# Kernel optimization log

Measured on AMD Instinct MI355X. Metric: run time of the kernel, lower is better.

## Reference

```python
import jax, jax.numpy as jnp
import numpy as np

B, D, E, H, L, T = 512, 64, 512, 1024, 2, 96
LN_EPS = 1e-5


def setup_inputs() -> dict:
    key = jax.random.key(0)
    ks = jax.random.split(key, 20)
    r = lambda k, shape, sc=0.05: (jax.random.normal(k, shape, jnp.float32) * sc)
    inp = {
        "x_0": jax.random.normal(ks[0], (B, D), jnp.float32),
        "h_n": jax.random.normal(ks[1], (L, B, H), jnp.float32) * 0.1,
        "c_n": jax.random.normal(ks[2], (L, B, H), jnp.float32) * 0.1,
        "forecast_window": T,
        # share_embedding: Linear(D -> E)
        "emb_W": r(ks[3], (D, E)),
        "emb_b": r(ks[4], (E,)),
        # LSTM layer 0: input E -> hidden H ; gates order (i, f, g, o)
        "W_ih0": r(ks[5], (E, 4 * H)),
        "W_hh0": r(ks[6], (H, 4 * H)),
        "b_ih0": r(ks[7], (4 * H,)),
        "b_hh0": r(ks[8], (4 * H,)),
        # LSTM layer 1: input H -> hidden H
        "W_ih1": r(ks[9], (H, 4 * H)),
        "W_hh1": r(ks[10], (H, 4 * H)),
        "b_ih1": r(ks[11], (4 * H,)),
        "b_hh1": r(ks[12], (4 * H,)),
        # fc: Linear(H,H) -> LayerNorm(H) -> ReLU -> Linear(H,D)
        "fc1_W": r(ks[13], (H, H)),
        "fc1_b": r(ks[14], (H,)),
        "ln_g": jnp.ones((H,), jnp.float32),
        "ln_b": jnp.zeros((H,), jnp.float32),
        "fc2_W": r(ks[15], (H, D)),
        "fc2_b": r(ks[16], (D,)),
    }
    return inp


def _lstm_cell(x, h, c, Wih, Whh, b):
    gates = x @ Wih + h @ Whh + b  # [B, 4H]
    i, f, g, o = jnp.split(gates, 4, axis=-1)
    c2 = jax.nn.sigmoid(f) * c + jax.nn.sigmoid(i) * jnp.tanh(g)
    h2 = jax.nn.sigmoid(o) * jnp.tanh(c2)
    return h2, c2


def reference(x_0, h_n, c_n, forecast_window, emb_W, emb_b,
              W_ih0, W_hh0, b_ih0, b_hh0, W_ih1, W_hh1, b_ih1, b_hh1,
              fc1_W, fc1_b, ln_g, ln_b, fc2_W, fc2_b):
    b0 = b_ih0 + b_hh0
    b1 = b_ih1 + b_hh1

    def step(carry, _):
        x, h0, c0, h1, c1 = carry
        xe = x @ emb_W + emb_b                      # embedding
        h0, c0 = _lstm_cell(xe, h0, c0, W_ih0, W_hh0, b0)
        h1, c1 = _lstm_cell(h0, h1, c1, W_ih1, W_hh1, b1)
        z = h1 @ fc1_W + fc1_b                      # Linear
        mu = jnp.mean(z, axis=-1, keepdims=True)    # LayerNorm
        var = jnp.mean((z - mu) ** 2, axis=-1, keepdims=True)
        z = (z - mu) * jax.lax.rsqrt(var + LN_EPS) * ln_g + ln_b
        y = jax.nn.relu(z) @ fc2_W + fc2_b          # ReLU -> Linear
        return (y, h0, c0, h1, c1), y

    carry0 = (x_0, h_n[0], c_n[0], h_n[1], c_n[1])
    _, ys = jax.lax.scan(step, carry0, None, length=int(forecast_window))
    return jnp.transpose(ys, (1, 0, 2))  # [B, T, D]
```

## Files before the change

kernel.cpp:

```cpp
#include <hip/hip_runtime.h>
#include <hip/hip_bf16.h>

using bf16 = __hip_bfloat16;
using short8 = __attribute__((ext_vector_type(8))) short;
using f32x4 = __attribute__((ext_vector_type(4))) float;

#define BB 512
#define HH 1024
#define DD 64
#define TT 96

__device__ __forceinline__ void load_lds16(const void* g, void* l) {
  __builtin_amdgcn_global_load_lds(
      (const __attribute__((address_space(1))) unsigned int*)g,
      (__attribute__((address_space(3))) unsigned int*)l, 16, 0, 0);
}

__device__ __forceinline__ float sigm(float x) { return 1.0f / (1.0f + __expf(-x)); }
__device__ __forceinline__ float tanh_f(float x) {
  float e = __expf(2.0f * x);
  return 1.0f - 2.0f / (e + 1.0f);
}
__device__ __forceinline__ float wred(float v) {
#pragma unroll
  for (int m = 1; m < 64; m <<= 1) v += __shfl_xor(v, m, 64);
  return v;
}


__global__ __launch_bounds__(256) void init_states_k(
    const float* __restrict__ x0, const float* __restrict__ hn, const float* __restrict__ cn,
    bf16* __restrict__ xbh, bf16* __restrict__ xbl,
    bf16* __restrict__ h0h, bf16* __restrict__ h0l,
    bf16* __restrict__ h1h, bf16* __restrict__ h1l,
    float* __restrict__ c0, float* __restrict__ c1)
{
  int i = blockIdx.x * 256 + threadIdx.x;
  if (i < BB * HH) {
    float v0 = hn[i];
    bf16 a0 = __float2bfloat16(v0);
    h0h[i] = a0; h0l[i] = __float2bfloat16(v0 - __bfloat162float(a0));
    float v1 = hn[BB * HH + i];
    bf16 a1 = __float2bfloat16(v1);
    h1h[i] = a1; h1l[i] = __float2bfloat16(v1 - __bfloat162float(a1));
    c0[i] = cn[i];
    c1[i] = cn[BB * HH + i];
  }
  if (i < BB * DD) {
    float v = x0[i];
    bf16 a = __float2bfloat16(v);
    xbh[i] = a; xbl[i] = __float2bfloat16(v - __bfloat162float(a));
  }
}

__device__ __forceinline__ int gate_perm(int c) {
  int g = c >> 10, n = c & 1023;
  return (n >> 5) * 128 + g * 32 + (n & 31);
}

__global__ __launch_bounds__(256) void fold_emb_k(
    const float* __restrict__ embW, const float* __restrict__ embB,
    const float* __restrict__ Wih0, const float* __restrict__ bih0, const float* __restrict__ bhh0,
    bf16* __restrict__ W0h, bf16* __restrict__ W0l, float* __restrict__ bias0)
{
  __shared__ float sW[512 * 8];
  __shared__ float sb[512];
  int tid = threadIdx.x;
  int d0 = blockIdx.y * 8;
  for (int i = tid; i < 4096; i += 256) {
    int j = i >> 9;
    int e = i & 511;
    sW[e * 8 + j] = embW[(size_t)(d0 + j) * 512 + e];
  }
  for (int i = tid; i < 512; i += 256) sb[i] = embB[i];
  __syncthreads();
  int c = blockIdx.x * 256 + tid;
  float acc[8] = {0, 0, 0, 0, 0, 0, 0, 0};
  float bacc = 0.0f;
  for (int e = 0; e < 512; ++e) {
    float wv = Wih0[(size_t)e * 4096 + c];
    float4 wa = *(const float4*)&sW[e * 8];
    float4 wb = *(const float4*)&sW[e * 8 + 4];
    acc[0] += wa.x * wv; acc[1] += wa.y * wv; acc[2] += wa.z * wv; acc[3] += wa.w * wv;
    acc[4] += wb.x * wv; acc[5] += wb.y * wv; acc[6] += wb.z * wv; acc[7] += wb.w * wv;
    bacc += sb[e] * wv;
  }
  int pr = gate_perm(c);
#pragma unroll
  for (int j = 0; j < 8; ++j) {
    float v = acc[j];
    bf16 h = __float2bfloat16(v);
    W0h[(size_t)pr * 1088 + d0 + j] = h;
    W0l[(size_t)pr * 1088 + d0 + j] = __float2bfloat16(v - __bfloat162float(h));
  }
  if (blockIdx.y == 0) bias0[pr] = bacc + bih0[c] + bhh0[c];
}

template <bool PERM>
__global__ __launch_bounds__(256) void transpose_conv_k(
    const float* __restrict__ src, int N,
    bf16* __restrict__ dsth, bf16* __restrict__ dstl, int dstStride, int k0)
{
  __shared__ float tb[32][33];
  int tx = threadIdx.x & 31;
  int ty = threadIdx.x >> 5;
  int c0 = blockIdx.x * 32;
  int kk0 = blockIdx.y * 32;
#pragma unroll
  for (int q = 0; q < 4; ++q) {
    int k = kk0 + q * 8 + ty;
    tb[q * 8 + ty][tx] = src[(size_t)k * N + c0 + tx];
  }
  __syncthreads();
#pragma unroll
  for (int q = 0; q < 4; ++q) {
    int cc = c0 + q * 8 + ty;
    int pr = PERM ? gate_perm(cc) : cc;
    float v = tb[tx][q * 8 + ty];
    bf16 h = __float2bfloat16(v);
    size_t di = (size_t)pr * dstStride + k0 + kk0 + tx;
    dsth[di] = h;
    dstl[di] = __float2bfloat16(v - __bfloat162float(h));
  }
}

__global__ __launch_bounds__(256) void bias_perm_k(
    const float* __restrict__ a, const float* __restrict__ b, float* __restrict__ out)
{
  int c = blockIdx.x * 256 + threadIdx.x;
  out[gate_perm(c)] = a[c] + b[c];
}

template <int EPI>
__global__ __launch_bounds__(256) void gemm_step_k(
    const bf16* __restrict__ A1h, const bf16* __restrict__ A1l, int lda1, int K1len,
    const bf16* __restrict__ A2h, const bf16* __restrict__ A2l, int lda2,
    const bf16* __restrict__ Bth, const bf16* __restrict__ Btl, int KTOT,
    const float* __restrict__ bias,
    float* __restrict__ zout,
    float* __restrict__ cstate,
    bf16* __restrict__ houth, bf16* __restrict__ houtl,
    int nPanels)
{
  __shared__ __align__(16) char smem[49152];
  const int tid = threadIdx.x;
  const int lane = tid & 63;
  const int wv = tid >> 6;
  const int bid = blockIdx.x;
  const int npanel = bid % nPanels;
  const int m0 = (bid / nPanels) * 64;
  const int nrow0 = npanel * 128;

  f32x4 acc[8] = {};
  const int ntiles = KTOT >> 5;

  auto stage = [&](int qbuf, int kt) {
    char* lb = smem + qbuf * 24576;
    {
      int row = tid >> 2, sl = tid & 3;
      int sb = (sl * 16) ^ (((row >> 2) & 3) << 4);
      int ke = kt + (sb >> 1);
      const bf16 *gh, *gl;
      if (kt < K1len) {
        gh = A1h + (size_t)(m0 + row) * lda1 + ke;
        gl = A1l + (size_t)(m0 + row) * lda1 + ke;
      } else {
        gh = A2h + (size_t)(m0 + row) * lda2 + (ke - K1len);
        gl = A2l + (size_t)(m0 + row) * lda2 + (ke - K1len);
      }
      load_lds16((const void*)gh, (void*)(lb + tid * 16));
      load_lds16((const void*)gl, (void*)(lb + 4096 + tid * 16));
    }
#pragma unroll
    for (int q = 0; q < 2; ++q) {
      int L = q * 256 + tid;
      int row = L >> 2, sl = L & 3;
      int sb = (sl * 16) ^ (((row >> 2) & 3) << 4);
      int ke = kt + (sb >> 1);
      load_lds16((const void*)(Bth + (size_t)(nrow0 + row) * KTOT + ke),
                 (void*)(lb + 8192 + L * 16));
      load_lds16((const void*)(Btl + (size_t)(nrow0 + row) * KTOT + ke),
                 (void*)(lb + 16384 + L * 16));
    }
  };

  stage(0, 0);
  __syncthreads();
  const int l15 = lane & 15;
  const int lhi = lane >> 4;
  const int kb = lhi * 16;
  const int arow = wv * 16 + l15;
  const int aoff = arow * 64 + (kb ^ (((arow >> 2) & 3) << 4));

  for (int t = 0; t < ntiles; ++t) {
    int cur = t & 1;
    if (t + 1 < ntiles) stage(cur ^ 1, (t + 1) << 5);
    const char* base = smem + cur * 24576;
    short8 ah = *(const short8*)(base + aoff);
    short8 al = *(const short8*)(base + 4096 + aoff);
#pragma unroll
    for (int f = 0; f < 8; ++f) {
      int brow = f * 16 + l15;
      int boff = brow * 64 + (kb ^ (((brow >> 2) & 3) << 4));
      short8 bh = *(const short8*)(base + 8192 + boff);
      short8 bl = *(const short8*)(base + 16384 + boff);
      acc[f] = __builtin_amdgcn_mfma_f32_16x16x32_bf16(ah, bh, acc[f], 0, 0, 0);
      acc[f] = __builtin_amdgcn_mfma_f32_16x16x32_bf16(ah, bl, acc[f], 0, 0, 0);
      acc[f] = __builtin_amdgcn_mfma_f32_16x16x32_bf16(al, bh, acc[f], 0, 0, 0);
    }
    __syncthreads();
  }

  if (EPI == 0) {
#pragma unroll
    for (int s = 0; s < 2; ++s) {
      f32x4 ai = acc[0 + s], af = acc[2 + s], ag = acc[4 + s], ao = acc[6 + s];
      int unit = npanel * 32 + s * 16 + l15;
      int prb = npanel * 128 + s * 16 + l15;
      float bi = bias[prb + 0];
      float bfv = bias[prb + 32];
      float bg = bias[prb + 64];
      float bo = bias[prb + 96];
#pragma unroll
      for (int r = 0; r < 4; ++r) {
        int row = m0 + wv * 16 + lhi * 4 + r;
        float iv = ai[r] + bi;
        float fv = af[r] + bfv;
        float gv = ag[r] + bg;
        float ov = ao[r] + bo;
        size_t idx = (size_t)row * HH + unit;
        float co = cstate[idx];
        float cn2 = sigm(fv) * co + sigm(iv) * tanh_f(gv);
        cstate[idx] = cn2;
        float hv = sigm(ov) * tanh_f(cn2);
        bf16 hh = __float2bfloat16(hv);
        houth[idx] = hh;
        houtl[idx] = __float2bfloat16(hv - __bfloat162float(hh));
      }
    }
  } else {
#pragma unroll
    for (int f = 0; f < 8; ++f) {
      int col = npanel * 128 + f * 16 + l15;
      float bb = bias[col];
#pragma unroll
      for (int r = 0; r < 4; ++r) {
        int row = m0 + wv * 16 + lhi * 4 + r;
        zout[(size_t)row * HH + col] = acc[f][r] + bb;
      }
    }
  }
}

__global__ __launch_bounds__(256) void ln_fc2_k(
    const float* __restrict__ z, const float* __restrict__ lng, const float* __restrict__ lnb,
    const float* __restrict__ W2 , const float* __restrict__ b2,
    float* __restrict__ out ,
    bf16* __restrict__ xbh, bf16* __restrict__ xbl, int tstep)
{
  __shared__ float sa[4][1024];
  __shared__ float red[4][4][64];
  int tid = threadIdx.x, lane = tid & 63, w = tid >> 6;
  int row = blockIdx.x * 4 + w;
  float zv[16];
#pragma unroll
  for (int j = 0; j < 16; ++j) zv[j] = z[(size_t)row * 1024 + j * 64 + lane];
  float s = 0;
#pragma unroll
  for (int j = 0; j < 16; ++j) s += zv[j];
  s = wred(s);
  float mu = s * (1.0f / 1024.0f);
  float vs = 0;
#pragma unroll
  for (int j = 0; j < 16; ++j) { float d = zv[j] - mu; vs += d * d; }
  vs = wred(vs);
  float rstd = rsqrtf(vs * (1.0f / 1024.0f) + 1e-5f);
#pragma unroll
  for (int j = 0; j < 16; ++j) {
    int k = j * 64 + lane;
    float a = (zv[j] - mu) * rstd * lng[k] + lnb[k];
    sa[w][k] = a > 0.0f ? a : 0.0f;
  }
  __syncthreads();
  int n = tid & 63, ks = (tid >> 6) * 256;
  float p0 = 0, p1 = 0, p2 = 0, p3 = 0;
  for (int k = ks; k < ks + 256; ++k) {
    float wv2 = W2[(size_t)k * 64 + n];
    p0 += sa[0][k] * wv2; p1 += sa[1][k] * wv2; p2 += sa[2][k] * wv2; p3 += sa[3][k] * wv2;
  }
  int sl = tid >> 6;
  red[0][sl][n] = p0; red[1][sl][n] = p1; red[2][sl][n] = p2; red[3][sl][n] = p3;
  __syncthreads();
  int rr = tid >> 6;
  float y = red[rr][0][n] + red[rr][1][n] + red[rr][2][n] + red[rr][3][n] + b2[n];
  int orow = blockIdx.x * 4 + rr;
  out[((size_t)orow * TT + tstep) * DD + n] = y;
  bf16 hh = __float2bfloat16(y);
  xbh[(size_t)orow * DD + n] = hh;
  xbl[(size_t)orow * DD + n] = __float2bfloat16(y - __bfloat162float(hh));
}


extern "C" void kernel_launch(void* const* d_in, const int* in_sizes, int n_in,
                              void* d_out, int out_size, void* d_ws, size_t ws_size,
                              hipStream_t stream)
{
  const float* x0   = (const float*)d_in[0];
  const float* hn   = (const float*)d_in[1];
  const float* cn   = (const float*)d_in[2];
  const float* embW = (const float*)d_in[4];
  const float* embB = (const float*)d_in[5];
  const float* Wih0 = (const float*)d_in[6];
  const float* Whh0 = (const float*)d_in[7];
  const float* bih0 = (const float*)d_in[8];
  const float* bhh0 = (const float*)d_in[9];
  const float* Wih1 = (const float*)d_in[10];
  const float* Whh1 = (const float*)d_in[11];
  const float* bih1 = (const float*)d_in[12];
  const float* bhh1 = (const float*)d_in[13];
  const float* fc1W = (const float*)d_in[14];
  const float* fc1b = (const float*)d_in[15];
  const float* lng  = (const float*)d_in[16];
  const float* lnb  = (const float*)d_in[17];
  const float* fc2W = (const float*)d_in[18];
  const float* fc2b = (const float*)d_in[19];

  char* wp = (char*)d_ws;
  size_t off = 0;
  auto alloc = [&](size_t bytes) -> void* {
    void* p = wp + off;
    off += (bytes + 255) & ~(size_t)255;
    return p;
  };

  bf16* W0th  = (bf16*)alloc((size_t)4096 * 1088 * 2);
  bf16* W0tl  = (bf16*)alloc((size_t)4096 * 1088 * 2);
  bf16* W1th  = (bf16*)alloc((size_t)4096 * 2048 * 2);
  bf16* W1tl  = (bf16*)alloc((size_t)4096 * 2048 * 2);
  bf16* f1h   = (bf16*)alloc((size_t)1024 * 1024 * 2);
  bf16* f1l   = (bf16*)alloc((size_t)1024 * 1024 * 2);
  float* bias0 = (float*)alloc(4096 * 4);
  float* bias1 = (float*)alloc(4096 * 4);
  bf16* xbh   = (bf16*)alloc((size_t)BB * DD * 2);
  bf16* xbl   = (bf16*)alloc((size_t)BB * DD * 2);
  bf16* h0h_a = (bf16*)alloc((size_t)BB * HH * 2);
  bf16* h0h_b = (bf16*)alloc((size_t)BB * HH * 2);
  bf16* h0l_a = (bf16*)alloc((size_t)BB * HH * 2);
  bf16* h0l_b = (bf16*)alloc((size_t)BB * HH * 2);
  bf16* h1h_a = (bf16*)alloc((size_t)BB * HH * 2);
  bf16* h1h_b = (bf16*)alloc((size_t)BB * HH * 2);
  bf16* h1l_a = (bf16*)alloc((size_t)BB * HH * 2);
  bf16* h1l_b = (bf16*)alloc((size_t)BB * HH * 2);
  float* c0   = (float*)alloc((size_t)BB * HH * 4);
  float* c1   = (float*)alloc((size_t)BB * HH * 4);
  float* z    = (float*)alloc((size_t)BB * HH * 4);

  init_states_k<<<2048, 256, 0, stream>>>(x0, hn, cn, xbh, xbl, h0h_a, h0l_a, h1h_a, h1l_a, c0, c1);
  fold_emb_k<<<dim3(16, 8), 256, 0, stream>>>(embW, embB, Wih0, bih0, bhh0, W0th, W0tl, bias0);
  transpose_conv_k<true><<<dim3(128, 32), 256, 0, stream>>>(Whh0, 4096, W0th, W0tl, 1088, 64);
  transpose_conv_k<true><<<dim3(128, 32), 256, 0, stream>>>(Wih1, 4096, W1th, W1tl, 2048, 0);
  transpose_conv_k<true><<<dim3(128, 32), 256, 0, stream>>>(Whh1, 4096, W1th, W1tl, 2048, 1024);
  transpose_conv_k<false><<<dim3(32, 32), 256, 0, stream>>>(fc1W, 1024, f1h, f1l, 1024, 0);
  bias_perm_k<<<16, 256, 0, stream>>>(bih1, bhh1, bias1);

  bf16* h0h[2] = {h0h_a, h0h_b};
  bf16* h0l[2] = {h0l_a, h0l_b};
  bf16* h1h[2] = {h1h_a, h1h_b};
  bf16* h1l[2] = {h1l_a, h1l_b};
  float* outp = (float*)d_out;

  for (int t = 0; t < TT; ++t) {
    int p = t & 1;
    gemm_step_k<0><<<256, 256, 0, stream>>>(
        xbh, xbl, DD, DD, h0h[p], h0l[p], HH, W0th, W0tl, 1088, bias0,
        nullptr, c0, h0h[p ^ 1], h0l[p ^ 1], 32);
    gemm_step_k<0><<<256, 256, 0, stream>>>(
        h0h[p ^ 1], h0l[p ^ 1], HH, HH, h1h[p], h1l[p], HH, W1th, W1tl, 2048, bias1,
        nullptr, c1, h1h[p ^ 1], h1l[p ^ 1], 32);
    gemm_step_k<1><<<64, 256, 0, stream>>>(
        h1h[p ^ 1], h1l[p ^ 1], HH, 1024, h1h[p ^ 1], h1l[p ^ 1], HH, f1h, f1l, 1024,
        fc1b, z, nullptr, nullptr, nullptr, 8);
    ln_fc2_k<<<128, 256, 0, stream>>>(z, lng, lnb, fc2W, fc2b, outp, xbh, xbl, t);
  }
}
```

Measured before the change: 10.72 ms.

## Replace per-step kernel launches with a persistent kernel using grid barriers

The 384 per-timestep launches (two LSTM gate GEMMs, fc1 GEMM, LayerNorm+fc2) are merged into one persistent kernel of 256 blocks of 128 threads. The phases are separated by a software global barrier built on atomics. The gate GEMM tiling changes to 4x4 MFMA fragments per wave, with a finer gate permutation (16-unit groups). fc1 and LN/fc2 are retiled so every phase uses the same 256 blocks. This removes launch and tail overhead, but the barrier requires all blocks to be co-resident and cuts per-block parallelism, with only 2 waves per block in most phases.

```diff
diff --git a/kernel.cpp b/kernel.cpp
--- a/kernel.cpp
+++ b/kernel.cpp
@@ -9,6 +9,7 @@
 #define HH 1024
 #define DD 64
 #define TT 96
+#define NBLK 256
 
 __device__ __forceinline__ void load_lds16(const void* g, void* l) {
   __builtin_amdgcn_global_load_lds(
@@ -25,6 +26,11 @@
 #pragma unroll
   for (int m = 1; m < 64; m <<= 1) v += __shfl_xor(v, m, 64);
   return v;
+}
+
+__device__ __forceinline__ int gate_perm(int c) {
+  int g = c >> 10, n = c & 1023;
+  return (n >> 4) * 64 + g * 16 + (n & 15);
 }
 
 
@@ -33,9 +39,10 @@
     bf16* __restrict__ xbh, bf16* __restrict__ xbl,
     bf16* __restrict__ h0h, bf16* __restrict__ h0l,
     bf16* __restrict__ h1h, bf16* __restrict__ h1l,
-    float* __restrict__ c0, float* __restrict__ c1)
+    float* __restrict__ c0, float* __restrict__ c1, unsigned* __restrict__ barp)
 {
   int i = blockIdx.x * 256 + threadIdx.x;
+  if (blockIdx.x == 0 && threadIdx.x < 128) barp[threadIdx.x] = 0u;
   if (i < BB * HH) {
     float v0 = hn[i];
     bf16 a0 = __float2bfloat16(v0);
@@ -51,11 +58,6 @@
     bf16 a = __float2bfloat16(v);
     xbh[i] = a; xbl[i] = __float2bfloat16(v - __bfloat162float(a));
   }
-}
-
-__device__ __forceinline__ int gate_perm(int c) {
-  int g = c >> 10, n = c & 1023;
-  return (n >> 5) * 128 + g * 32 + (n & 31);
 }
 
 __global__ __launch_bounds__(256) void fold_emb_k(
@@ -131,140 +133,232 @@
   out[gate_perm(c)] = a[c] + b[c];
 }
 
-template <int EPI>
-__global__ __launch_bounds__(256) void gemm_step_k(
-    const bf16* __restrict__ A1h, const bf16* __restrict__ A1l, int lda1, int K1len,
-    const bf16* __restrict__ A2h, const bf16* __restrict__ A2l, int lda2,
-    const bf16* __restrict__ Bth, const bf16* __restrict__ Btl, int KTOT,
-    const float* __restrict__ bias,
-    float* __restrict__ zout,
-    float* __restrict__ cstate,
-    bf16* __restrict__ houth, bf16* __restrict__ houtl,
-    int nPanels)
-{
-  __shared__ __align__(16) char smem[49152];
-  const int tid = threadIdx.x;
-  const int lane = tid & 63;
-  const int wv = tid >> 6;
-  const int bid = blockIdx.x;
-  const int npanel = bid % nPanels;
-  const int m0 = (bid / nPanels) * 64;
+
+struct PA {
+  bf16 *xbh, *xbl;
+  bf16 *h0h_a, *h0h_b, *h0l_a, *h0l_b;
+  bf16 *h1h_a, *h1h_b, *h1l_a, *h1l_b;
+  float *c0, *c1, *z;
+  const bf16 *W0h, *W0l, *W1h, *W1l, *F1h, *F1l;
+  const float *bias0, *bias1, *fc1b, *lng, *lnb, *W2, *b2;
+  float *out;
+  unsigned *bar;
+};
+
+__device__ __forceinline__ void gbar(unsigned* bar, int tid) {
+  __syncthreads();
+  if (tid == 0) {
+    __threadfence();
+    unsigned* gen = bar + 64;
+    unsigned g = __hip_atomic_load(gen, __ATOMIC_RELAXED, __HIP_MEMORY_SCOPE_AGENT);
+    unsigned a = __hip_atomic_fetch_add(bar, 1u, __ATOMIC_ACQ_REL, __HIP_MEMORY_SCOPE_AGENT);
+    if (a == NBLK - 1) {
+      __hip_atomic_store(bar, 0u, __ATOMIC_RELAXED, __HIP_MEMORY_SCOPE_AGENT);
+      __hip_atomic_store(gen, g + 1u, __ATOMIC_RELEASE, __HIP_MEMORY_SCOPE_AGENT);
+    } else {
+      while (__hip_atomic_load(gen, __ATOMIC_ACQUIRE, __HIP_MEMORY_SCOPE_AGENT) == g)
+        __builtin_amdgcn_s_sleep(2);
+    }
+  }
+  __syncthreads();
+}
+
+__device__ __forceinline__ void gates_phase(
+    char* smem, int bid, int tid,
+    const bf16* A1h, const bf16* A1l, int lda1, int K1len,
+    const bf16* A2h, const bf16* A2l, int lda2,
+    const bf16* Bh, const bf16* Bl, int KTOT,
+    const float* bias, float* cst, bf16* hho, bf16* hlo)
+{
+  const int lane = tid & 63, wv = tid >> 6;
+  const int npanel = bid & 31, m0 = (bid >> 5) * 64;
   const int nrow0 = npanel * 128;
-
-  f32x4 acc[8] = {};
+  const int l15 = lane & 15, lhi = lane >> 4, kb = lhi * 16;
+
+  f32x4 acc[16];
+#pragma unroll
+  for (int i = 0; i < 16; ++i) acc[i] = f32x4{0, 0, 0, 0};
+
   const int ntiles = KTOT >> 5;
 
-  auto stage = [&](int qbuf, int kt) {
-    char* lb = smem + qbuf * 24576;
+  auto stage = [&](int buf, int kt) {
+    char* lb = smem + buf * 24576;
+    bool first = kt < K1len;
+#pragma unroll
+    for (int q = 0; q < 2; ++q) {
+      int L = q * 128 + tid;
+      int row = L >> 2, sl = L & 3;
+      int sb = (sl * 16) ^ (((row >> 2) & 3) << 4);
+      int ke = kt + (sb >> 1);
+      const bf16* gh = first ? A1h + (size_t)(m0 + row) * lda1 + ke
+                             : A2h + (size_t)(m0 + row) * lda2 + (ke - K1len);
+      const bf16* gl = first ? A1l + (size_t)(m0 + row) * lda1 + ke
+                             : A2l + (size_t)(m0 + row) * lda2 + (ke - K1len);
+      load_lds16(gh, lb + L * 16);
+      load_lds16(gl, lb + 4096 + L * 16);
+    }
+#pragma unroll
+    for (int q = 0; q < 4; ++q) {
+      int L = q * 128 + tid;
+      int row = L >> 2, sl = L & 3;
+      int sb = (sl * 16) ^ (((row >> 2) & 3) << 4);
+      int ke = kt + (sb >> 1);
+      load_lds16(Bh + (size_t)(nrow0 + row) * KTOT + ke, lb + 8192 + L * 16);
+      load_lds16(Bl + (size_t)(nrow0 + row) * KTOT + ke, lb + 16384 + L * 16);
+    }
+  };
+
+  stage(0, 0);
+  __syncthreads();
+  for (int t = 0; t < ntiles; ++t) {
+    int cur = t & 1;
+    if (t + 1 < ntiles) stage(cur ^ 1, (t + 1) << 5);
+    const char* base = smem + cur * 24576;
+    short8 ah[4], al[4], bh[4], bl[4];
+#pragma unroll
+    for (int mf = 0; mf < 4; ++mf) {
+      int arow = mf * 16 + l15;
+      int aoff = arow * 64 + (kb ^ (((arow >> 2) & 3) << 4));
+      ah[mf] = *(const short8*)(base + aoff);
+      al[mf] = *(const short8*)(base + 4096 + aoff);
+    }
+#pragma unroll
+    for (int nf = 0; nf < 4; ++nf) {
+      int brow = wv * 64 + nf * 16 + l15;
+      int boff = brow * 64 + (kb ^ (((brow >> 2) & 3) << 4));
+      bh[nf] = *(const short8*)(base + 8192 + boff);
+      bl[nf] = *(const short8*)(base + 16384 + boff);
+    }
+#pragma unroll
+    for (int mf = 0; mf < 4; ++mf)
+#pragma unroll
+      for (int nf = 0; nf < 4; ++nf) {
+        f32x4 c = acc[mf * 4 + nf];
+        c = __builtin_amdgcn_mfma_f32_16x16x32_bf16(ah[mf], bh[nf], c, 0, 0, 0);
+        c = __builtin_amdgcn_mfma_f32_16x16x32_bf16(ah[mf], bl[nf], c, 0, 0, 0);
+        c = __builtin_amdgcn_mfma_f32_16x16x32_bf16(al[mf], bh[nf], c, 0, 0, 0);
+        acc[mf * 4 + nf] = c;
+      }
+    __syncthreads();
+  }
+
+  const int unit = npanel * 32 + wv * 16 + l15;
+  const int prb = npanel * 128 + wv * 64 + l15;
+  float bi = bias[prb + 0];
+  float bfv = bias[prb + 16];
+  float bg = bias[prb + 32];
+  float bo = bias[prb + 48];
+#pragma unroll
+  for (int mf = 0; mf < 4; ++mf) {
+    f32x4 ai = acc[mf * 4 + 0], af = acc[mf * 4 + 1];
+    f32x4 ag = acc[mf * 4 + 2], ao = acc[mf * 4 + 3];
+#pragma unroll
+    for (int r = 0; r < 4; ++r) {
+      int row = m0 + mf * 16 + lhi * 4 + r;
+      size_t idx = (size_t)row * HH + unit;
+      float iv = ai[r] + bi, fv = af[r] + bfv, gv = ag[r] + bg, ov = ao[r] + bo;
+      float co = cst[idx];
+      float cn2 = sigm(fv) * co + sigm(iv) * tanh_f(gv);
+      cst[idx] = cn2;
+      float hv = sigm(ov) * tanh_f(cn2);
+      bf16 hh = __float2bfloat16(hv);
+      hho[idx] = hh;
+      hlo[idx] = __float2bfloat16(hv - __bfloat162float(hh));
+    }
+  }
+}
+
+__device__ __forceinline__ void fc1_phase(
+    char* smem, int bid, int tid,
+    const bf16* Ah, const bf16* Al,
+    const bf16* Bh, const bf16* Bl,
+    const float* bias, float* z)
+{
+  const int lane = tid & 63, wv = tid >> 6;
+  const int n0 = (bid & 15) * 64, m0 = (bid >> 4) * 32;
+  const int l15 = lane & 15, lhi = lane >> 4, kb = lhi * 16;
+  f32x4 acc[4];
+#pragma unroll
+  for (int i = 0; i < 4; ++i) acc[i] = f32x4{0, 0, 0, 0};
+
+  auto stage = [&](int buf, int kt) {
+    char* lb = smem + buf * 12288;
     {
       int row = tid >> 2, sl = tid & 3;
       int sb = (sl * 16) ^ (((row >> 2) & 3) << 4);
       int ke = kt + (sb >> 1);
-      const bf16 *gh, *gl;
-      if (kt < K1len) {
-        gh = A1h + (size_t)(m0 + row) * lda1 + ke;
-        gl = A1l + (size_t)(m0 + row) * lda1 + ke;
-      } else {
-        gh = A2h + (size_t)(m0 + row) * lda2 + (ke - K1len);
-        gl = A2l + (size_t)(m0 + row) * lda2 + (ke - K1len);
-      }
-      load_lds16((const void*)gh, (void*)(lb + tid * 16));
-      load_lds16((const void*)gl, (void*)(lb + 4096 + tid * 16));
+      load_lds16(Ah + (size_t)(m0 + row) * HH + ke, lb + tid * 16);
+      load_lds16(Al + (size_t)(m0 + row) * HH + ke, lb + 2048 + tid * 16);
     }
 #pragma unroll
     for (int q = 0; q < 2; ++q) {
-      int L = q * 256 + tid;
+      int L = q * 128 + tid;
       int row = L >> 2, sl = L & 3;
       int sb = (sl * 16) ^ (((row >> 2) & 3) << 4);
       int ke = kt + (sb >> 1);
-      load_lds16((const void*)(Bth + (size_t)(nrow0 + row) * KTOT + ke),
-                 (void*)(lb + 8192 + L * 16));
-      load_lds16((const void*)(Btl + (size_t)(nrow0 + row) * KTOT + ke),
-                 (void*)(lb + 16384 + L * 16));
+      load_lds16(Bh + (size_t)(n0 + row) * HH + ke, lb + 4096 + L * 16);
+      load_lds16(Bl + (size_t)(n0 + row) * HH + ke, lb + 8192 + L * 16);
     }
   };
-
   stage(0, 0);
   __syncthreads();
-  const int l15 = lane & 15;
-  const int lhi = lane >> 4;
-  const int kb = lhi * 16;
-  const int arow = wv * 16 + l15;
-  const int aoff = arow * 64 + (kb ^ (((arow >> 2) & 3) << 4));
-
-  for (int t = 0; t < ntiles; ++t) {
+  for (int t = 0; t < 32; ++t) {
     int cur = t & 1;
-    if (t + 1 < ntiles) stage(cur ^ 1, (t + 1) << 5);
-    const char* base = smem + cur * 24576;
-    short8 ah = *(const short8*)(base + aoff);
-    short8 al = *(const short8*)(base + 4096 + aoff);
-#pragma unroll
-    for (int f = 0; f < 8; ++f) {
-      int brow = f * 16 + l15;
+    if (t + 1 < 32) stage(cur ^ 1, (t + 1) << 5);
+    const char* base = smem + cur * 12288;
+    short8 ah[2], al[2], bh[2], bl[2];
+#pragma unroll
+    for (int mf = 0; mf < 2; ++mf) {
+      int arow = mf * 16 + l15;
+      int aoff = arow * 64 + (kb ^ (((arow >> 2) & 3) << 4));
+      ah[mf] = *(const short8*)(base + aoff);
+      al[mf] = *(const short8*)(base + 2048 + aoff);
+    }
+#pragma unroll
+    for (int nf = 0; nf < 2; ++nf) {
+      int brow = wv * 32 + nf * 16 + l15;
       int boff = brow * 64 + (kb ^ (((brow >> 2) & 3) << 4));
-      short8 bh = *(const short8*)(base + 8192 + boff);
-      short8 bl = *(const short8*)(base + 16384 + boff);
-      acc[f] = __builtin_amdgcn_mfma_f32_16x16x32_bf16(ah, bh, acc[f], 0, 0, 0);
-      acc[f] = __builtin_amdgcn_mfma_f32_16x16x32_bf16(ah, bl, acc[f], 0, 0, 0);
-      acc[f] = __builtin_amdgcn_mfma_f32_16x16x32_bf16(al, bh, acc[f], 0, 0, 0);
-    }
+      bh[nf] = *(const short8*)(base + 4096 + boff);
+      bl[nf] = *(const short8*)(base + 8192 + boff);
+    }
+#pragma unroll
+    for (int mf = 0; mf < 2; ++mf)
+#pragma unroll
+      for (int nf = 0; nf < 2; ++nf) {
+        f32x4 c = acc[mf * 2 + nf];
+        c = __builtin_amdgcn_mfma_f32_16x16x32_bf16(ah[mf], bh[nf], c, 0, 0, 0);
+        c = __builtin_amdgcn_mfma_f32_16x16x32_bf16(ah[mf], bl[nf], c, 0, 0, 0);
+        c = __builtin_amdgcn_mfma_f32_16x16x32_bf16(al[mf], bh[nf], c, 0, 0, 0);
+        acc[mf * 2 + nf] = c;
+      }
     __syncthreads();
   }
-
-  if (EPI == 0) {
-#pragma unroll
-    for (int s = 0; s < 2; ++s) {
-      f32x4 ai = acc[0 + s], af = acc[2 + s], ag = acc[4 + s], ao = acc[6 + s];
-      int unit = npanel * 32 + s * 16 + l15;
-      int prb = npanel * 128 + s * 16 + l15;
-      float bi = bias[prb + 0];
-      float bfv = bias[prb + 32];
-      float bg = bias[prb + 64];
-      float bo = bias[prb + 96];
+#pragma unroll
+  for (int mf = 0; mf < 2; ++mf)
+#pragma unroll
+    for (int nf = 0; nf < 2; ++nf) {
+      int col = n0 + wv * 32 + nf * 16 + l15;
+      float bb = bias[col];
 #pragma unroll
       for (int r = 0; r < 4; ++r) {
-        int row = m0 + wv * 16 + lhi * 4 + r;
-        float iv = ai[r] + bi;
-        float fv = af[r] + bfv;
-        float gv = ag[r] + bg;
-        float ov = ao[r] + bo;
-        size_t idx = (size_t)row * HH + unit;
-        float co = cstate[idx];
-        float cn2 = sigm(fv) * co + sigm(iv) * tanh_f(gv);
-        cstate[idx] = cn2;
-        float hv = sigm(ov) * tanh_f(cn2);
-        bf16 hh = __float2bfloat16(hv);
-        houth[idx] = hh;
-        houtl[idx] = __float2bfloat16(hv - __bfloat162float(hh));
+        int row = m0 + mf * 16 + lhi * 4 + r;
+        z[(size_t)row * HH + col] = acc[mf * 2 + nf][r] + bb;
       }
     }
-  } else {
-#pragma unroll
-    for (int f = 0; f < 8; ++f) {
-      int col = npanel * 128 + f * 16 + l15;
-      float bb = bias[col];
-#pragma unroll
-      for (int r = 0; r < 4; ++r) {
-        int row = m0 + wv * 16 + lhi * 4 + r;
-        zout[(size_t)row * HH + col] = acc[f][r] + bb;
-      }
-    }
-  }
-}
-
-__global__ __launch_bounds__(256) void ln_fc2_k(
-    const float* __restrict__ z, const float* __restrict__ lng, const float* __restrict__ lnb,
-    const float* __restrict__ W2 , const float* __restrict__ b2,
-    float* __restrict__ out ,
-    bf16* __restrict__ xbh, bf16* __restrict__ xbl, int tstep)
-{
-  __shared__ float sa[4][1024];
-  __shared__ float red[4][4][64];
-  int tid = threadIdx.x, lane = tid & 63, w = tid >> 6;
-  int row = blockIdx.x * 4 + w;
+}
+
+__device__ __forceinline__ void ln_phase(
+    char* smem, int bid, int tid,
+    const float* z, const float* lng, const float* lnb,
+    const float* W2, const float* b2,
+    float* out, bf16* xbh, bf16* xbl, int tstep)
+{
+  float* sa = (float*)smem;
+  const int lane = tid & 63, wv = tid >> 6;
+  const int row = bid * 2 + wv;
   float zv[16];
 #pragma unroll
-  for (int j = 0; j < 16; ++j) zv[j] = z[(size_t)row * 1024 + j * 64 + lane];
+  for (int j = 0; j < 16; ++j) zv[j] = z[(size_t)row * HH + j * 64 + lane];
   float s = 0;
 #pragma unroll
   for (int j = 0; j < 16; ++j) s += zv[j];
@@ -278,26 +372,43 @@
 #pragma unroll
   for (int j = 0; j < 16; ++j) {
     int k = j * 64 + lane;
-    float a = (zv[j] - mu) * rstd * lng[k] + lnb[k];
-    sa[w][k] = a > 0.0f ? a : 0.0f;
-  }
-  __syncthreads();
-  int n = tid & 63, ks = (tid >> 6) * 256;
-  float p0 = 0, p1 = 0, p2 = 0, p3 = 0;
-  for (int k = ks; k < ks + 256; ++k) {
-    float wv2 = W2[(size_t)k * 64 + n];
-    p0 += sa[0][k] * wv2; p1 += sa[1][k] * wv2; p2 += sa[2][k] * wv2; p3 += sa[3][k] * wv2;
-  }
-  int sl = tid >> 6;
-  red[0][sl][n] = p0; red[1][sl][n] = p1; red[2][sl][n] = p2; red[3][sl][n] = p3;
-  __syncthreads();
-  int rr = tid >> 6;
-  float y = red[rr][0][n] + red[rr][1][n] + red[rr][2][n] + red[rr][3][n] + b2[n];
-  int orow = blockIdx.x * 4 + rr;
-  out[((size_t)orow * TT + tstep) * DD + n] = y;
+    float a2 = (zv[j] - mu) * rstd * lng[k] + lnb[k];
+    sa[wv * 1024 + k] = a2 > 0.0f ? a2 : 0.0f;
+  }
+  __syncthreads();
+  float y = b2[lane];
+#pragma unroll 8
+  for (int k = 0; k < 1024; ++k)
+    y += sa[wv * 1024 + k] * W2[(size_t)k * DD + lane];
+  out[((size_t)row * TT + tstep) * DD + lane] = y;
   bf16 hh = __float2bfloat16(y);
-  xbh[(size_t)orow * DD + n] = hh;
-  xbl[(size_t)orow * DD + n] = __float2bfloat16(y - __bfloat162float(hh));
+  xbh[(size_t)row * DD + lane] = hh;
+  xbl[(size_t)row * DD + lane] = __float2bfloat16(y - __bfloat162float(hh));
+}
+
+__global__ __launch_bounds__(128) void persistent_k(PA a)
+{
+  __shared__ __align__(16) char smem[49152];
+  const int tid = threadIdx.x, bid = blockIdx.x;
+  bf16 *h0hp = a.h0h_a, *h0hc = a.h0h_b, *h0lp = a.h0l_a, *h0lc = a.h0l_b;
+  bf16 *h1hp = a.h1h_a, *h1hc = a.h1h_b, *h1lp = a.h1l_a, *h1lc = a.h1l_b;
+  for (int t = 0; t < TT; ++t) {
+    gates_phase(smem, bid, tid, a.xbh, a.xbl, DD, DD, h0hp, h0lp, HH,
+                a.W0h, a.W0l, 1088, a.bias0, a.c0, h0hc, h0lc);
+    gbar(a.bar, tid);
+    gates_phase(smem, bid, tid, h0hc, h0lc, HH, HH, h1hp, h1lp, HH,
+                a.W1h, a.W1l, 2048, a.bias1, a.c1, h1hc, h1lc);
+    gbar(a.bar, tid);
+    fc1_phase(smem, bid, tid, h1hc, h1lc, a.F1h, a.F1l, a.fc1b, a.z);
+    gbar(a.bar, tid);
+    ln_phase(smem, bid, tid, a.z, a.lng, a.lnb, a.W2, a.b2, a.out, a.xbh, a.xbl, t);
+    gbar(a.bar, tid);
+    bf16* tmp;
+    tmp = h0hp; h0hp = h0hc; h0hc = tmp;
+    tmp = h0lp; h0lp = h0lc; h0lc = tmp;
+    tmp = h1hp; h1hp = h1hc; h1hc = tmp;
+    tmp = h1lp; h1lp = h1lc; h1lc = tmp;
+  }
 }
 
 
@@ -354,8 +465,10 @@
   float* c0   = (float*)alloc((size_t)BB * HH * 4);
   float* c1   = (float*)alloc((size_t)BB * HH * 4);
   float* z    = (float*)alloc((size_t)BB * HH * 4);
-
-  init_states_k<<<2048, 256, 0, stream>>>(x0, hn, cn, xbh, xbl, h0h_a, h0l_a, h1h_a, h1l_a, c0, c1);
+  unsigned* bar = (unsigned*)alloc(512);
+
+  init_states_k<<<2048, 256, 0, stream>>>(x0, hn, cn, xbh, xbl, h0h_a, h0l_a,
+                                          h1h_a, h1l_a, c0, c1, bar);
   fold_emb_k<<<dim3(16, 8), 256, 0, stream>>>(embW, embB, Wih0, bih0, bhh0, W0th, W0tl, bias0);
   transpose_conv_k<true><<<dim3(128, 32), 256, 0, stream>>>(Whh0, 4096, W0th, W0tl, 1088, 64);
   transpose_conv_k<true><<<dim3(128, 32), 256, 0, stream>>>(Wih1, 4096, W1th, W1tl, 2048, 0);
@@ -363,23 +476,17 @@
   transpose_conv_k<false><<<dim3(32, 32), 256, 0, stream>>>(fc1W, 1024, f1h, f1l, 1024, 0);
   bias_perm_k<<<16, 256, 0, stream>>>(bih1, bhh1, bias1);
 
-  bf16* h0h[2] = {h0h_a, h0h_b};
-  bf16* h0l[2] = {h0l_a, h0l_b};
-  bf16* h1h[2] = {h1h_a, h1h_b};
-  bf16* h1l[2] = {h1l_a, h1l_b};
-  float* outp = (float*)d_out;
-
-  for (int t = 0; t < TT; ++t) {
-    int p = t & 1;
-    gemm_step_k<0><<<256, 256, 0, stream>>>(
-        xbh, xbl, DD, DD, h0h[p], h0l[p], HH, W0th, W0tl, 1088, bias0,
-        nullptr, c0, h0h[p ^ 1], h0l[p ^ 1], 32);
-    gemm_step_k<0><<<256, 256, 0, stream>>>(
-        h0h[p ^ 1], h0l[p ^ 1], HH, HH, h1h[p], h1l[p], HH, W1th, W1tl, 2048, bias1,
-        nullptr, c1, h1h[p ^ 1], h1l[p ^ 1], 32);
-    gemm_step_k<1><<<64, 256, 0, stream>>>(
-        h1h[p ^ 1], h1l[p ^ 1], HH, 1024, h1h[p ^ 1], h1l[p ^ 1], HH, f1h, f1l, 1024,
-        fc1b, z, nullptr, nullptr, nullptr, 8);
-    ln_fc2_k<<<128, 256, 0, stream>>>(z, lng, lnb, fc2W, fc2b, outp, xbh, xbl, t);
-  }
-}
+  PA pa;
+  pa.xbh = xbh; pa.xbl = xbl;
+  pa.h0h_a = h0h_a; pa.h0h_b = h0h_b; pa.h0l_a = h0l_a; pa.h0l_b = h0l_b;
+  pa.h1h_a = h1h_a; pa.h1h_b = h1h_b; pa.h1l_a = h1l_a; pa.h1l_b = h1l_b;
+  pa.c0 = c0; pa.c1 = c1; pa.z = z;
+  pa.W0h = W0th; pa.W0l = W0tl; pa.W1h = W1th; pa.W1l = W1tl;
+  pa.F1h = f1h; pa.F1l = f1l;
+  pa.bias0 = bias0; pa.bias1 = bias1; pa.fc1b = fc1b;
+  pa.lng = lng; pa.lnb = lnb; pa.W2 = fc2W; pa.b2 = fc2b;
+  pa.out = (float*)d_out;
+  pa.bar = bar;
+
+  persistent_k<<<NBLK, 128, 0, stream>>>(pa);
+}
```

After: 40.61 ms. 279% more time.
